# Optimization experiments

Hardware: AMD Instinct MI355X
Metric: run time of the kernel (lower is better)

The kernel has to match this reference:

```python
import jax, jax.numpy as jnp
import numpy as np

NUM_HEADS = 16
D_ATT = 64


def setup_inputs() -> dict:
    key = jax.random.key(0)
    ks = jax.random.split(key, 7)
    b, n, hd = 4, 2048, NUM_HEADS * 64  # input last dim = num_heads * per-head embed_dim
    Q_vec = jax.random.normal(ks[0], (b, n, hd), dtype=jnp.float32)
    K_vec = jax.random.normal(ks[1], (b, n, hd), dtype=jnp.float32)
    V_vec = jax.random.normal(ks[2], (b, n, hd), dtype=jnp.float32)
    # torch Linear weights: [out_features, in_features] = [d_attention, per_head_dim]
    W_Q = jax.random.normal(ks[3], (D_ATT, 64), dtype=jnp.float32) * 0.02
    W_K = jax.random.normal(ks[4], (D_ATT, 64), dtype=jnp.float32) * 0.02
    W_V = jax.random.normal(ks[5], (D_ATT, 64), dtype=jnp.float32) * 0.02
    mask = jax.random.bernoulli(ks[6], p=0.9, shape=(b, n))  # bool [b, n]
    return {"Q_vec": Q_vec, "K_vec": K_vec, "V_vec": V_vec,
            "W_Q": W_Q, "W_K": W_K, "W_V": W_V, "mask": mask}


def reference(Q_vec, K_vec, V_vec, W_Q, W_K, W_V, mask):
    b, n, _ = Q_vec.shape
    h = NUM_HEADS
    scaling = 1.0 / np.sqrt(D_ATT).astype(np.float32)

    def split_heads(x):  # b n (h d) -> b h n d
        return x.reshape(b, n, h, -1).transpose(0, 2, 1, 3)

    # Linear applied per-head (weights are [out, in]; y = x @ W^T)
    q = split_heads(Q_vec) @ W_Q.T  # [b,h,n,D_ATT]
    k = split_heads(K_vec) @ W_K.T
    v = split_heads(V_vec) @ W_V.T

    dots = jnp.einsum('bhid,bhjd->bhij', q, k) * scaling  # [b,h,n,n]
    pair_mask = mask[:, None, :] & mask[:, :, None]       # [b,n,n]
    mask_value = -jnp.finfo(dots.dtype).max
    dots = jnp.where(pair_mask[:, None, :, :], dots, mask_value)
    attn = jax.nn.softmax(dots, axis=-1)
    out = jnp.einsum('bhij,bhjd->bhid', attn, v)          # [b,h,n,D_ATT]
    return out.transpose(0, 2, 1, 3).reshape(b, n, h * D_ATT)
```

## Files before the change

### kernel.cpp

```cpp
#include <hip/hip_runtime.h>

#define B_  4
#define N_  2048
#define H_  16
#define HD_ 1024

typedef short  bf16x8 __attribute__((ext_vector_type(8)));
typedef short  bf16x4 __attribute__((ext_vector_type(4)));
typedef float  f32x4  __attribute__((ext_vector_type(4)));

static __device__ __forceinline__ unsigned short f2bf(float f) {
    unsigned int u = __builtin_bit_cast(unsigned int, f);
    u += 0x7FFFu + ((u >> 16) & 1u);
    return (unsigned short)(u >> 16);
}

static __device__ __forceinline__ unsigned rne_hi(float f) {
    unsigned u = __builtin_bit_cast(unsigned, f);
    return u + 0x7FFFu + ((u >> 16) & 1u);
}
static __device__ __forceinline__ unsigned f2bf2pack(float lo, float hi) {
    return __builtin_amdgcn_perm(rne_hi(hi), rne_hi(lo), 0x07060302u);
}

__global__ __launch_bounds__(256) void proj_kernel(
    const float* __restrict__ Qv, const float* __restrict__ Kv,
    const float* __restrict__ Vv, const float* __restrict__ WQ,
    const float* __restrict__ WK, const float* __restrict__ WV,
    unsigned short* __restrict__ qs, unsigned short* __restrict__ ks,
    unsigned short* __restrict__ vt)
{
    __shared__ __align__(16) unsigned short xb[64][72];
    __shared__ __align__(16) unsigned short Wb[64][72];
    __shared__ __align__(16) unsigned short sb[64][72];

    const int tid  = threadIdx.x;
    const int wq   = tid >> 6;
    const int lane = tid & 63;
    const int l15  = lane & 15;
    const int quad = lane >> 4;

    const int i0 = blockIdx.x * 64;
    const int h  = blockIdx.y;
    const int bz = blockIdx.z;
    const int b  = bz / 3;
    const int p  = bz - b * 3;

    const size_t inbase = ((size_t)b * N_ + i0) * HD_ + h * 64;
    const size_t bh     = (size_t)b * H_ + h;

    const float* W   = (p == 0) ? WQ : (p == 1) ? WK : WV;
    const float* inp = ((p == 0) ? Qv : (p == 1) ? Kv : Vv) + inbase;

    for (int v = tid; v < 1024; v += 256) {
        int tok = v >> 4, c4 = (v & 15) * 4;
        float4 f = *reinterpret_cast<const float4*>(inp + (size_t)tok * HD_ + c4);
        uint2 u;
        u.x = f2bf2pack(f.x, f.y);
        u.y = f2bf2pack(f.z, f.w);
        *reinterpret_cast<uint2*>(&xb[tok][c4]) = u;
        float4 g = *reinterpret_cast<const float4*>(W + (size_t)v * 4);
        uint2 w2;
        w2.x = f2bf2pack(g.x, g.y);
        w2.y = f2bf2pack(g.z, g.w);
        *reinterpret_cast<uint2*>(&Wb[tok][c4]) = w2;
    }
    __syncthreads();

    bf16x8 ax[2];
    #pragma unroll
    for (int kh = 0; kh < 2; ++kh)
        ax[kh] = *reinterpret_cast<const bf16x8*>(&xb[wq * 16 + l15][kh * 32 + quad * 8]);

    f32x4 C[4];
    #pragma unroll
    for (int t = 0; t < 4; ++t) {
        C[t] = f32x4{0.f, 0.f, 0.f, 0.f};
        #pragma unroll
        for (int kh = 0; kh < 2; ++kh) {
            bf16x8 bw = *reinterpret_cast<const bf16x8*>(&Wb[t * 16 + l15][kh * 32 + quad * 8]);
            C[t] = __builtin_amdgcn_mfma_f32_16x16x32_bf16(ax[kh], bw, C[t], 0, 0, 0);
        }
    }

    if (p < 2) {
        const float scl = (p == 0) ? 0.180336880f : 1.f;
        #pragma unroll
        for (int t = 0; t < 4; ++t)
            #pragma unroll
            for (int r = 0; r < 4; ++r)
                sb[wq * 16 + quad * 4 + r][t * 16 + l15] = f2bf(C[t][r] * scl);
        __syncthreads();
        unsigned short* dst = ((p == 0) ? qs : ks) + ((size_t)bh * N_ + i0) * 64;
        for (int v = tid; v < 512; v += 256) {
            int row = v >> 3, c0 = (v & 7) * 8;
            *reinterpret_cast<uint4*>(dst + (size_t)row * 64 + c0) =
                *reinterpret_cast<const uint4*>(&sb[row][c0]);
        }
    } else {
        #pragma unroll
        for (int t = 0; t < 4; ++t) {
            uint2 u;
            u.x = f2bf2pack(C[t][0], C[t][1]);
            u.y = f2bf2pack(C[t][2], C[t][3]);
            *reinterpret_cast<uint2*>(&sb[t * 16 + l15][wq * 16 + quad * 4]) = u;
        }
        __syncthreads();
        unsigned short* vdst = vt + (size_t)bh * 64 * N_ + i0;
        for (int v = tid; v < 512; v += 256) {
            int d = v >> 3, c0 = (v & 7) * 8;
            *reinterpret_cast<uint4*>(vdst + (size_t)d * N_ + c0) =
                *reinterpret_cast<const uint4*>(&sb[d][c0]);
        }
    }
}

__global__ __launch_bounds__(256, 2) void attn_kernel(
    const unsigned short* __restrict__ qs, const unsigned short* __restrict__ ks,
    const unsigned short* __restrict__ vt, const int* __restrict__ maskp,
    float* __restrict__ out)
{
    __shared__ __align__(16) unsigned short Ks[64][72];
    __shared__ __align__(16) unsigned short Vt[64][68];
    __shared__ float kb[64];

    const int tid  = threadIdx.x;
    const int w    = tid >> 6;
    const int lane = tid & 63;
    const int l15  = lane & 15;
    const int quad = lane >> 4;

    const int i0 = blockIdx.x * 256;
    const int bh = blockIdx.y;
    const int b  = bh >> 4;
    const int h  = bh & 15;
    const int qrow0 = i0 + w * 64;

    bf16x8 aq[4][2];
    float  qm[4];
    #pragma unroll
    for (int rt = 0; rt < 4; ++rt) {
        const unsigned short* qrow = qs + ((size_t)bh * N_ + qrow0 + rt * 16 + l15) * 64;
        aq[rt][0] = *reinterpret_cast<const bf16x8*>(qrow + quad * 8);
        aq[rt][1] = *reinterpret_cast<const bf16x8*>(qrow + 32 + quad * 8);
        qm[rt] = maskp[b * N_ + qrow0 + rt * 16 + l15] ? 1.f : 0.f;
    }

    bf16x8 aones;
    #pragma unroll
    for (int j = 0; j < 8; ++j) aones[j] = (short)0x3F80;

    f32x4 O[4][4];
    f32x4 L[4];
    #pragma unroll
    for (int rt = 0; rt < 4; ++rt) {
        L[rt] = f32x4{0.f, 0.f, 0.f, 0.f};
        #pragma unroll
        for (int c = 0; c < 4; ++c) O[rt][c] = f32x4{0.f, 0.f, 0.f, 0.f};
    }

    const unsigned short* kbase = ks + (size_t)bh * N_ * 64;
    const unsigned short* vbase = vt + (size_t)bh * 64 * N_;

    for (int kv0 = 0; kv0 < N_; kv0 += 64) {
        __syncthreads();
        #pragma unroll
        for (int it = 0; it < 2; ++it) {
            int idx = tid + it * 256;
            int r = idx >> 3, g = idx & 7;
            *reinterpret_cast<uint4*>(&Ks[r][g * 8]) =
                *reinterpret_cast<const uint4*>(kbase + (size_t)(kv0 + r) * 64 + g * 8);
        }
        #pragma unroll
        for (int it = 0; it < 4; ++it) {
            int idx = tid + it * 256;
            int r = idx >> 4, g2 = idx & 15;
            *reinterpret_cast<uint2*>(&Vt[r][g2 * 4]) =
                *reinterpret_cast<const uint2*>(vbase + (size_t)r * N_ + kv0 + g2 * 4);
        }
        if (tid < 64) kb[tid] = maskp[b * N_ + kv0 + tid] ? 0.f : -1e30f;
        __syncthreads();

        bf16x8 ak[4][2];
        #pragma unroll
        for (int ct = 0; ct < 4; ++ct)
            #pragma unroll
            for (int kh = 0; kh < 2; ++kh)
                ak[ct][kh] = *reinterpret_cast<const bf16x8*>(&Ks[ct * 16 + l15][kh * 32 + quad * 8]);

        bf16x8 av[4][2];
        #pragma unroll
        for (int ct = 0; ct < 4; ++ct)
            #pragma unroll
            for (int kh = 0; kh < 2; ++kh) {
                bf16x4 lo = *reinterpret_cast<const bf16x4*>(&Vt[ct * 16 + l15][kh * 32 + quad * 4]);
                bf16x4 hi = *reinterpret_cast<const bf16x4*>(&Vt[ct * 16 + l15][kh * 32 + 16 + quad * 4]);
                av[ct][kh] = bf16x8{lo[0], lo[1], lo[2], lo[3], hi[0], hi[1], hi[2], hi[3]};
            }

        f32x4 kbv[4];
        #pragma unroll
        for (int ct = 0; ct < 4; ++ct)
            kbv[ct] = *reinterpret_cast<const f32x4*>(&kb[ct * 16 + quad * 4]);

        #pragma unroll
        for (int rt = 0; rt < 4; ++rt) {
            f32x4 S[4];
            #pragma unroll
            for (int ct = 0; ct < 4; ++ct) {
                S[ct] = f32x4{0.f, 0.f, 0.f, 0.f};
                #pragma unroll
                for (int kh = 0; kh < 2; ++kh)
                    S[ct] = __builtin_amdgcn_mfma_f32_16x16x32_bf16(ak[ct][kh], aq[rt][kh], S[ct], 0, 0, 0);
            }
            unsigned pk[4][2];
            #pragma unroll
            for (int ct = 0; ct < 4; ++ct) {
                float e0 = __builtin_amdgcn_exp2f((S[ct][0] + kbv[ct][0]) * qm[rt]);
                float e1 = __builtin_amdgcn_exp2f((S[ct][1] + kbv[ct][1]) * qm[rt]);
                float e2 = __builtin_amdgcn_exp2f((S[ct][2] + kbv[ct][2]) * qm[rt]);
                float e3 = __builtin_amdgcn_exp2f((S[ct][3] + kbv[ct][3]) * qm[rt]);
                pk[ct][0] = f2bf2pack(e0, e1);
                pk[ct][1] = f2bf2pack(e2, e3);
            }
            bf16x8 ap[2];
            #pragma unroll
            for (int kh = 0; kh < 2; ++kh) {
                uint4 u = uint4{pk[2 * kh][0], pk[2 * kh][1], pk[2 * kh + 1][0], pk[2 * kh + 1][1]};
                ap[kh] = __builtin_bit_cast(bf16x8, u);
            }
            #pragma unroll
            for (int kh = 0; kh < 2; ++kh)
                L[rt] = __builtin_amdgcn_mfma_f32_16x16x32_bf16(aones, ap[kh], L[rt], 0, 0, 0);
            #pragma unroll
            for (int ct = 0; ct < 4; ++ct)
                #pragma unroll
                for (int kh = 0; kh < 2; ++kh)
                    O[rt][ct] = __builtin_amdgcn_mfma_f32_16x16x32_bf16(av[ct][kh], ap[kh], O[rt][ct], 0, 0, 0);
        }
    }

    #pragma unroll
    for (int rt = 0; rt < 4; ++rt) {
        float inv = 1.f / L[rt][0];
        float* orow = out + ((size_t)b * N_ + qrow0 + rt * 16 + l15) * HD_ + h * 64 + quad * 4;
        #pragma unroll
        for (int ct = 0; ct < 4; ++ct)
            #pragma unroll
            for (int r = 0; r < 4; ++r)
                orow[ct * 16 + r] = O[rt][ct][r] * inv;
    }
}

extern "C" void kernel_launch(void* const* d_in, const int* in_sizes, int n_in,
                              void* d_out, int out_size, void* d_ws, size_t ws_size,
                              hipStream_t stream)
{
    const float* Qv  = (const float*)d_in[0];
    const float* Kv  = (const float*)d_in[1];
    const float* Vv  = (const float*)d_in[2];
    const float* WQ  = (const float*)d_in[3];
    const float* WK  = (const float*)d_in[4];
    const float* WV  = (const float*)d_in[5];
    const int*   msk = (const int*)d_in[6];
    float* out = (float*)d_out;

    const size_t per = (size_t)B_ * H_ * N_ * 64;
    unsigned short* qsb = (unsigned short*)d_ws;
    unsigned short* ksb = qsb + per;
    unsigned short* vtb = ksb + per;

    proj_kernel<<<dim3(N_ / 64, H_, B_ * 3), 256, 0, stream>>>(Qv, Kv, Vv, WQ, WK, WV, qsb, ksb, vtb);
    attn_kernel<<<dim3(N_ / 256, B_ * H_), 256, 0, stream>>>(qsb, ksb, vtb, msk, out);
}
```

Baseline: 245.0 us.

## Rewrite projection to use register-resident weights and shrink attention query tile

```diff
diff --git a/kernel.cpp b/kernel.cpp
--- a/kernel.cpp
+++ b/kernel.cpp
@@ -9,18 +9,22 @@
 typedef short  bf16x4 __attribute__((ext_vector_type(4)));
 typedef float  f32x4  __attribute__((ext_vector_type(4)));
 
-static __device__ __forceinline__ unsigned short f2bf(float f) {
-    unsigned int u = __builtin_bit_cast(unsigned int, f);
-    u += 0x7FFFu + ((u >> 16) & 1u);
-    return (unsigned short)(u >> 16);
-}
-
 static __device__ __forceinline__ unsigned rne_hi(float f) {
     unsigned u = __builtin_bit_cast(unsigned, f);
     return u + 0x7FFFu + ((u >> 16) & 1u);
 }
 static __device__ __forceinline__ unsigned f2bf2pack(float lo, float hi) {
     return __builtin_amdgcn_perm(rne_hi(hi), rne_hi(lo), 0x07060302u);
+}
+static __device__ __forceinline__ bf16x8 cvt8(const float* p) {
+    float4 f0 = *reinterpret_cast<const float4*>(p);
+    float4 f1 = *reinterpret_cast<const float4*>(p + 4);
+    uint4 u;
+    u.x = f2bf2pack(f0.x, f0.y);
+    u.y = f2bf2pack(f0.z, f0.w);
+    u.z = f2bf2pack(f1.x, f1.y);
+    u.w = f2bf2pack(f1.z, f1.w);
+    return __builtin_bit_cast(bf16x8, u);
 }
 
 __global__ __launch_bounds__(256) void proj_kernel(
@@ -30,92 +34,73 @@
     unsigned short* __restrict__ qs, unsigned short* __restrict__ ks,
     unsigned short* __restrict__ vt)
 {
-    __shared__ __align__(16) unsigned short xb[64][72];
-    __shared__ __align__(16) unsigned short Wb[64][72];
-    __shared__ __align__(16) unsigned short sb[64][72];
-
     const int tid  = threadIdx.x;
-    const int wq   = tid >> 6;
+    const int w    = tid >> 6;
     const int lane = tid & 63;
     const int l15  = lane & 15;
     const int quad = lane >> 4;
 
-    const int i0 = blockIdx.x * 64;
+    const int i0 = blockIdx.x * 256;
     const int h  = blockIdx.y;
     const int bz = blockIdx.z;
     const int b  = bz / 3;
     const int p  = bz - b * 3;
 
-    const size_t inbase = ((size_t)b * N_ + i0) * HD_ + h * 64;
-    const size_t bh     = (size_t)b * H_ + h;
-
+    const size_t bh = (size_t)b * H_ + h;
     const float* W   = (p == 0) ? WQ : (p == 1) ? WK : WV;
-    const float* inp = ((p == 0) ? Qv : (p == 1) ? Kv : Vv) + inbase;
-
-    for (int v = tid; v < 1024; v += 256) {
-        int tok = v >> 4, c4 = (v & 15) * 4;
-        float4 f = *reinterpret_cast<const float4*>(inp + (size_t)tok * HD_ + c4);
-        uint2 u;
-        u.x = f2bf2pack(f.x, f.y);
-        u.y = f2bf2pack(f.z, f.w);
-        *reinterpret_cast<uint2*>(&xb[tok][c4]) = u;
-        float4 g = *reinterpret_cast<const float4*>(W + (size_t)v * 4);
-        uint2 w2;
-        w2.x = f2bf2pack(g.x, g.y);
-        w2.y = f2bf2pack(g.z, g.w);
-        *reinterpret_cast<uint2*>(&Wb[tok][c4]) = w2;
-    }
-    __syncthreads();
-
-    bf16x8 ax[2];
-    #pragma unroll
-    for (int kh = 0; kh < 2; ++kh)
-        ax[kh] = *reinterpret_cast<const bf16x8*>(&xb[wq * 16 + l15][kh * 32 + quad * 8]);
-
-    f32x4 C[4];
-    #pragma unroll
-    for (int t = 0; t < 4; ++t) {
-        C[t] = f32x4{0.f, 0.f, 0.f, 0.f};
-        #pragma unroll
-        for (int kh = 0; kh < 2; ++kh) {
-            bf16x8 bw = *reinterpret_cast<const bf16x8*>(&Wb[t * 16 + l15][kh * 32 + quad * 8]);
-            C[t] = __builtin_amdgcn_mfma_f32_16x16x32_bf16(ax[kh], bw, C[t], 0, 0, 0);
-        }
-    }
+    const float* X   = (p == 0) ? Qv : (p == 1) ? Kv : Vv;
+    const int tok0   = i0 + w * 64;
+
+    bf16x8 aw[4][2];
+    #pragma unroll
+    for (int mt = 0; mt < 4; ++mt)
+        #pragma unroll
+        for (int kh = 0; kh < 2; ++kh)
+            aw[mt][kh] = cvt8(W + (size_t)(16 * mt + l15) * 64 + kh * 32 + quad * 8);
 
     if (p < 2) {
         const float scl = (p == 0) ? 0.180336880f : 1.f;
-        #pragma unroll
-        for (int t = 0; t < 4; ++t)
-            #pragma unroll
-            for (int r = 0; r < 4; ++r)
-                sb[wq * 16 + quad * 4 + r][t * 16 + l15] = f2bf(C[t][r] * scl);
-        __syncthreads();
-        unsigned short* dst = ((p == 0) ? qs : ks) + ((size_t)bh * N_ + i0) * 64;
-        for (int v = tid; v < 512; v += 256) {
-            int row = v >> 3, c0 = (v & 7) * 8;
-            *reinterpret_cast<uint4*>(dst + (size_t)row * 64 + c0) =
-                *reinterpret_cast<const uint4*>(&sb[row][c0]);
+        unsigned short* dst = ((p == 0) ? qs : ks) + (size_t)bh * N_ * 64;
+        #pragma unroll
+        for (int g = 0; g < 4; ++g) {
+            const int tok = tok0 + g * 16 + l15;
+            const float* xrow = X + ((size_t)b * N_ + tok) * HD_ + h * 64;
+            bf16x8 bx[2] = {cvt8(xrow + quad * 8), cvt8(xrow + 32 + quad * 8)};
+            #pragma unroll
+            for (int mt = 0; mt < 4; ++mt) {
+                f32x4 C = f32x4{0.f, 0.f, 0.f, 0.f};
+                #pragma unroll
+                for (int kh = 0; kh < 2; ++kh)
+                    C = __builtin_amdgcn_mfma_f32_16x16x32_bf16(aw[mt][kh], bx[kh], C, 0, 0, 0);
+                uint2 u;
+                u.x = f2bf2pack(C[0] * scl, C[1] * scl);
+                u.y = f2bf2pack(C[2] * scl, C[3] * scl);
+                *reinterpret_cast<uint2*>(dst + (size_t)tok * 64 + 16 * mt + 4 * quad) = u;
+            }
         }
     } else {
-        #pragma unroll
-        for (int t = 0; t < 4; ++t) {
-            uint2 u;
-            u.x = f2bf2pack(C[t][0], C[t][1]);
-            u.y = f2bf2pack(C[t][2], C[t][3]);
-            *reinterpret_cast<uint2*>(&sb[t * 16 + l15][wq * 16 + quad * 4]) = u;
-        }
-        __syncthreads();
-        unsigned short* vdst = vt + (size_t)bh * 64 * N_ + i0;
-        for (int v = tid; v < 512; v += 256) {
-            int d = v >> 3, c0 = (v & 7) * 8;
-            *reinterpret_cast<uint4*>(vdst + (size_t)d * N_ + c0) =
-                *reinterpret_cast<const uint4*>(&sb[d][c0]);
-        }
-    }
-}
-
-__global__ __launch_bounds__(256, 2) void attn_kernel(
+        unsigned short* vdst = vt + (size_t)bh * 64 * N_;
+        #pragma unroll
+        for (int g = 0; g < 4; ++g) {
+            const int tokr = tok0 + g * 16 + l15;
+            const float* xrow = X + ((size_t)b * N_ + tokr) * HD_ + h * 64;
+            bf16x8 ax[2] = {cvt8(xrow + quad * 8), cvt8(xrow + 32 + quad * 8)};
+            #pragma unroll
+            for (int nt = 0; nt < 4; ++nt) {
+                f32x4 C = f32x4{0.f, 0.f, 0.f, 0.f};
+                #pragma unroll
+                for (int kh = 0; kh < 2; ++kh)
+                    C = __builtin_amdgcn_mfma_f32_16x16x32_bf16(ax[kh], aw[nt][kh], C, 0, 0, 0);
+                uint2 u;
+                u.x = f2bf2pack(C[0], C[1]);
+                u.y = f2bf2pack(C[2], C[3]);
+                *reinterpret_cast<uint2*>(vdst + (size_t)(16 * nt + l15) * N_ + tok0 + g * 16 + 4 * quad) = u;
+            }
+        }
+    }
+}
+
+__global__ __launch_bounds__(256, 4) void attn_kernel(
     const unsigned short* __restrict__ qs, const unsigned short* __restrict__ ks,
     const unsigned short* __restrict__ vt, const int* __restrict__ maskp,
     float* __restrict__ out)
@@ -130,16 +115,16 @@
     const int l15  = lane & 15;
     const int quad = lane >> 4;
 
-    const int i0 = blockIdx.x * 256;
+    const int i0 = blockIdx.x * 128;
     const int bh = blockIdx.y;
     const int b  = bh >> 4;
     const int h  = bh & 15;
-    const int qrow0 = i0 + w * 64;
-
-    bf16x8 aq[4][2];
-    float  qm[4];
-    #pragma unroll
-    for (int rt = 0; rt < 4; ++rt) {
+    const int qrow0 = i0 + w * 32;
+
+    bf16x8 aq[2][2];
+    float  qm[2];
+    #pragma unroll
+    for (int rt = 0; rt < 2; ++rt) {
         const unsigned short* qrow = qs + ((size_t)bh * N_ + qrow0 + rt * 16 + l15) * 64;
         aq[rt][0] = *reinterpret_cast<const bf16x8*>(qrow + quad * 8);
         aq[rt][1] = *reinterpret_cast<const bf16x8*>(qrow + 32 + quad * 8);
@@ -150,10 +135,10 @@
     #pragma unroll
     for (int j = 0; j < 8; ++j) aones[j] = (short)0x3F80;
 
-    f32x4 O[4][4];
-    f32x4 L[4];
-    #pragma unroll
-    for (int rt = 0; rt < 4; ++rt) {
+    f32x4 O[2][4];
+    f32x4 L[2];
+    #pragma unroll
+    for (int rt = 0; rt < 2; ++rt) {
         L[rt] = f32x4{0.f, 0.f, 0.f, 0.f};
         #pragma unroll
         for (int c = 0; c < 4; ++c) O[rt][c] = f32x4{0.f, 0.f, 0.f, 0.f};
@@ -204,7 +189,7 @@
             kbv[ct] = *reinterpret_cast<const f32x4*>(&kb[ct * 16 + quad * 4]);
 
         #pragma unroll
-        for (int rt = 0; rt < 4; ++rt) {
+        for (int rt = 0; rt < 2; ++rt) {
             f32x4 S[4];
             #pragma unroll
             for (int ct = 0; ct < 4; ++ct) {
@@ -241,7 +226,7 @@
     }
 
     #pragma unroll
-    for (int rt = 0; rt < 4; ++rt) {
+    for (int rt = 0; rt < 2; ++rt) {
         float inv = 1.f / L[rt][0];
         float* orow = out + ((size_t)b * N_ + qrow0 + rt * 16 + l15) * HD_ + h * 64 + quad * 4;
         #pragma unroll
@@ -270,6 +255,6 @@
     unsigned short* ksb = qsb + per;
     unsigned short* vtb = ksb + per;
 
-    proj_kernel<<<dim3(N_ / 64, H_, B_ * 3), 256, 0, stream>>>(Qv, Kv, Vv, WQ, WK, WV, qsb, ksb, vtb);
-    attn_kernel<<<dim3(N_ / 256, B_ * H_), 256, 0, stream>>>(qsb, ksb, vtb, msk, out);
-}
+    proj_kernel<<<dim3(N_ / 256, H_, B_ * 3), 256, 0, stream>>>(Qv, Kv, Vv, WQ, WK, WV, qsb, ksb, vtb);
+    attn_kernel<<<dim3(N_ / 128, B_ * H_), 256, 0, stream>>>(qsb, ksb, vtb, msk, out);
+}
```

New measurement: 558.1 us. +127.8%, slower.
